# Kernel optimization log

Measured on AMD Instinct MI355X. Metric: run time of the kernel, lower is better.

## Reference

```python
import jax, jax.numpy as jnp
import numpy as np

N = 8192        # nodes
D_IN = 512      # input features
H = 256         # hidden (GAT out_features)
D_OUT = 16      # output classes
K = 16          # num clusters/classes
LRELU_SLOPE = 0.2
MASK_FILL = -9e15
EDGE_P = 0.002  # sparsity of random adjacency


def setup_inputs() -> dict:
    key = jax.random.key(0)
    k1, k2, k3, k4, k5, k6 = jax.random.split(key, 6)
    x = jax.random.normal(k1, (N, D_IN), dtype=jnp.float32)
    # binary adjacency with self loops (module only tests adj > 0; support reused as propagation matrix)
    adj = (jax.random.uniform(k2, (N, N)) < EDGE_P).astype(jnp.float32)
    adj = jnp.maximum(adj, jnp.eye(N, dtype=jnp.float32))
    C_a = jax.random.normal(k3, (K, H), dtype=jnp.float32)
    # learned parameters (xavier-ish scale)
    W = jax.random.normal(k4, (D_IN, H), dtype=jnp.float32) * (1.414 * (2.0 / (D_IN + H)) ** 0.5)
    a = jax.random.normal(k5, (2 * H, 1), dtype=jnp.float32) * (1.414 * (2.0 / (2 * H + 1)) ** 0.5)
    W_gcn = jax.random.normal(k6, (H, D_OUT), dtype=jnp.float32)
    return {"x": x, "adj": adj, "C_a": C_a, "W": W, "a": a, "W_gcn": W_gcn}


def _clust_score(Z, C):
    # score[n,k] = exp(-||Z_n - C_k||) normalized over k (beta = 1)
    d = jnp.sqrt(((Z[:, None, :] - C[None, :, :]) ** 2).sum(-1))  # [N,K]
    s = jnp.exp(-d) + 1e-10
    return s / s.sum(axis=1, keepdims=True)


def reference(x, adj, C_a, W, a, W_gcn):
    h = W.shape[1]
    # --- GAT layer ---
    Wh = x @ W                                   # [N,H]
    Wh1 = Wh @ a[:h, :]                          # [N,1]
    Wh2 = Wh @ a[h:, :]                          # [N,1]
    e = jax.nn.leaky_relu(Wh1 + Wh2.T, LRELU_SLOPE)   # [N,N]
    att = jax.nn.softmax(jnp.where(adj > 0, e, MASK_FILL), axis=1)
    Z_0 = att @ Wh                               # h_prime, [N,H]
    gatoutput = jax.nn.elu(Z_0)
    # --- cluster score on detached Z_0 (update=False path) ---
    score = _clust_score(jax.lax.stop_gradient(Z_0), C_a)
    # --- GCN layer (B_1 = I, so Z_1 = F_1) ---
    F_1 = jax.nn.relu(adj @ (gatoutput @ W_gcn))  # [N,D_OUT]
    output = F_1
    Z_1 = F_1
    return (output, Z_1, Z_0, score)
```

## Files before the change

kernel.cpp:

```cpp
#include <hip/hip_runtime.h>
#include <hip/hip_bf16.h>

#define N_NODES 8192
#define D_IN    512
#define H       256
#define D_OUT   16
#define K_CL    16
#define MAXN    96

#define OUT_OFF 0
#define Z1_OFF  131072
#define Z0_OFF  262144
#define SC_OFF  2359296

typedef unsigned int   u32;
typedef unsigned short u16;
typedef __attribute__((ext_vector_type(8))) short bf16x8;
typedef __attribute__((ext_vector_type(4))) float f32x4;

__device__ __forceinline__ float load_in(const void* p, int bf, size_t idx) {
    if (bf) { u32 w = ((const u16*)p)[idx]; return __uint_as_float(w << 16); }
    return ((const float*)p)[idx];
}
__device__ __forceinline__ void store_out(void* p, int bf, size_t idx, float v) {
    if (bf) ((__hip_bfloat16*)p)[idx] = __float2bfloat16(v);
    else    ((float*)p)[idx] = v;
}

__global__ void k_detect(const u32* __restrict__ adjw, int* __restrict__ flag) {
    int t = blockIdx.x * 256 + threadIdx.x;
    int hit = 0;
    #pragma unroll 4
    for (int i = 0; i < 16; i++)
        if (adjw[(size_t)t + (size_t)i * 65536] == 0x00003F80u) hit = 1;
    if (hit) atomicOr(flag, 1);
}

__global__ void k_prep_small(const void* av, const void* C_a, const void* Wgcn,
                             const int* __restrict__ flag,
                             float* a_f, float* Ca_f, float* Wg_f) {
    int bf = *flag;
    int i = blockIdx.x * 256 + threadIdx.x;
    if (i < 512)        a_f[i]         = load_in(av,   bf, i);
    else if (i < 4608)  Ca_f[i - 512]  = load_in(C_a,  bf, i - 512);
    else if (i < 8704)  Wg_f[i - 4608] = load_in(Wgcn, bf, i - 4608);
}

__global__ void k_prep_wt(const void* __restrict__ wraw,
                          const int* __restrict__ flag, u16* __restrict__ Wt) {
    int bf = *flag;
    int idx = blockIdx.x * 256 + threadIdx.x;
    int h = idx >> 9, k = idx & 511;
    float v = load_in(wraw, bf, (size_t)k * H + h);
    __hip_bfloat16 b = __float2bfloat16(v);
    Wt[(size_t)h * D_IN + k] = *(u16*)&b;
}

__global__ __launch_bounds__(256) void k_gemm_wh(
    const void* __restrict__ xraw, const void* __restrict__ wraw,
    const u16* __restrict__ Wt,
    const int* __restrict__ flag, float* __restrict__ Wh)
{
    int bf = *flag;
    __shared__ float xs[32][68];
    __shared__ float ws_[32][68];
    int tid = threadIdx.x;
    int bm = blockIdx.x >> 2, bn = blockIdx.x & 3;
    int m0 = bm * 64, n0 = bn * 64;

    if (bf) {
        int wave = tid >> 6, lane = tid & 63;
        int wr = wave >> 1, wc = wave & 1;
        int r0 = m0 + wr * 32, c0 = n0 + wc * 32;
        int lr = lane & 15, lk = lane >> 4;
        const u16* xp = (const u16*)xraw;
        const u16* a0p = xp + (size_t)(r0 + lr)      * D_IN + lk * 8;
        const u16* a1p = xp + (size_t)(r0 + 16 + lr) * D_IN + lk * 8;
        const u16* b0p = Wt + (size_t)(c0 + lr)      * D_IN + lk * 8;
        const u16* b1p = Wt + (size_t)(c0 + 16 + lr) * D_IN + lk * 8;
        f32x4 acc[2][2] = {};
        #pragma unroll 4
        for (int k0 = 0; k0 < D_IN; k0 += 32) {
            bf16x8 a0 = *(const bf16x8*)(a0p + k0);
            bf16x8 a1 = *(const bf16x8*)(a1p + k0);
            bf16x8 b0 = *(const bf16x8*)(b0p + k0);
            bf16x8 b1 = *(const bf16x8*)(b1p + k0);
            acc[0][0] = __builtin_amdgcn_mfma_f32_16x16x32_bf16(a0, b0, acc[0][0], 0, 0, 0);
            acc[0][1] = __builtin_amdgcn_mfma_f32_16x16x32_bf16(a0, b1, acc[0][1], 0, 0, 0);
            acc[1][0] = __builtin_amdgcn_mfma_f32_16x16x32_bf16(a1, b0, acc[1][0], 0, 0, 0);
            acc[1][1] = __builtin_amdgcn_mfma_f32_16x16x32_bf16(a1, b1, acc[1][1], 0, 0, 0);
        }
        #pragma unroll
        for (int i = 0; i < 2; i++) {
            #pragma unroll
            for (int reg = 0; reg < 4; reg++) {
                int r = r0 + 16 * i + 4 * lk + reg;
                Wh[(size_t)r * H + c0 + lr]      = acc[i][0][reg];
                Wh[(size_t)r * H + c0 + 16 + lr] = acc[i][1][reg];
            }
        }
        return;
    }

    int tx = tid & 15, ty = tid >> 4;
    float acc[4][4] = {};
    for (int k0 = 0; k0 < D_IN; k0 += 32) {
        {
            int r = tid >> 2, kq = (tid & 3) * 8;
            size_t base = (size_t)(m0 + r) * D_IN + k0 + kq;
            float4 f0 = *(const float4*)((const float*)xraw + base);
            float4 f1 = *(const float4*)((const float*)xraw + base + 4);
            xs[kq + 0][r] = f0.x; xs[kq + 1][r] = f0.y;
            xs[kq + 2][r] = f0.z; xs[kq + 3][r] = f0.w;
            xs[kq + 4][r] = f1.x; xs[kq + 5][r] = f1.y;
            xs[kq + 6][r] = f1.z; xs[kq + 7][r] = f1.w;
        }
        {
            int kk = tid >> 3, n8 = (tid & 7) * 8;
            size_t base = (size_t)(k0 + kk) * H + n0 + n8;
            float4 f0 = *(const float4*)((const float*)wraw + base);
            float4 f1 = *(const float4*)((const float*)wraw + base + 4);
            ws_[kk][n8+0]=f0.x; ws_[kk][n8+1]=f0.y; ws_[kk][n8+2]=f0.z; ws_[kk][n8+3]=f0.w;
            ws_[kk][n8+4]=f1.x; ws_[kk][n8+5]=f1.y; ws_[kk][n8+6]=f1.z; ws_[kk][n8+7]=f1.w;
        }
        __syncthreads();
        #pragma unroll
        for (int kk = 0; kk < 32; kk++) {
            float4 a4 = *(const float4*)&xs[kk][ty * 4];
            float4 b4 = *(const float4*)&ws_[kk][tx * 4];
            float a[4] = {a4.x, a4.y, a4.z, a4.w};
            float b[4] = {b4.x, b4.y, b4.z, b4.w};
            #pragma unroll
            for (int i = 0; i < 4; i++)
                #pragma unroll
                for (int j = 0; j < 4; j++)
                    acc[i][j] += a[i] * b[j];
        }
        __syncthreads();
    }
    #pragma unroll
    for (int i = 0; i < 4; i++) {
        float4 o = {acc[i][0], acc[i][1], acc[i][2], acc[i][3]};
        *(float4*)&Wh[(size_t)(m0 + ty*4 + i) * H + n0 + tx*4] = o;
    }
}

__global__ __launch_bounds__(256) void k_wh12(
    const float* __restrict__ Wh, const float* __restrict__ a_f,
    float* __restrict__ Wh1, float* __restrict__ Wh2)
{
    int tid = threadIdx.x;
    int wave = tid >> 6, lane = tid & 63;
    int n = blockIdx.x * 4 + wave;
    float4 v  = *(const float4*)(Wh + (size_t)n * H + lane * 4);
    float4 a1 = *(const float4*)(a_f + lane * 4);
    float4 a2 = *(const float4*)(a_f + H + lane * 4);
    float s1 = v.x*a1.x + v.y*a1.y + v.z*a1.z + v.w*a1.w;
    float s2 = v.x*a2.x + v.y*a2.y + v.z*a2.z + v.w*a2.w;
    #pragma unroll
    for (int off = 32; off; off >>= 1) {
        s1 += __shfl_xor(s1, off);
        s2 += __shfl_xor(s2, off);
    }
    if (lane == 0) { Wh1[n] = s1; Wh2[n] = s2; }
}

__global__ __launch_bounds__(256) void k_gat_row(
    const void* __restrict__ adjraw, const int* __restrict__ flag,
    const float* __restrict__ Wh,
    const float* __restrict__ Wh1, const float* __restrict__ Wh2,
    const float* __restrict__ Ca_f, const float* __restrict__ Wg_f,
    float* __restrict__ Gf,
    int* __restrict__ nbr_cnt, u16* __restrict__ nbr_idx,
    void* __restrict__ dout)
{
    const int n = blockIdx.x;
    const int tid = threadIdx.x;
    const int bf = *flag;
    __shared__ int   s_cnt;
    __shared__ int   s_idx[MAXN];
    __shared__ float s_att[MAXN];
    __shared__ float s_z[H];
    __shared__ float s_g[H];
    __shared__ float s_red[256];
    __shared__ float s_sc[16];

    if (tid == 0) s_cnt = 0;
    __syncthreads();

    if (bf) {
        const u16* arow = (const u16*)adjraw + (size_t)n * N_NODES;
        #pragma unroll
        for (int it = 0; it < 4; it++) {
            int base = it * 2048 + tid * 8;
            uint4 raw = *(const uint4*)(arow + base);
            u32 rw[4] = {raw.x, raw.y, raw.z, raw.w};
            #pragma unroll
            for (int q = 0; q < 4; q++) {
                #pragma unroll
                for (int hh = 0; hh < 2; hh++) {
                    u32 u = (rw[q] >> (16 * hh)) & 0xFFFFu;
                    if (__uint_as_float(u << 16) > 0.f) {
                        int p = atomicAdd(&s_cnt, 1);
                        if (p < MAXN) s_idx[p] = base + q * 2 + hh;
                    }
                }
            }
        }
    } else {
        const float* arow = (const float*)adjraw + (size_t)n * N_NODES;
        #pragma unroll
        for (int it = 0; it < 8; it++) {
            int base = it * 1024 + tid * 4;
            float4 v = *(const float4*)(arow + base);
            float vv[4] = {v.x, v.y, v.z, v.w};
            #pragma unroll
            for (int q = 0; q < 4; q++) {
                if (vv[q] > 0.f) {
                    int p = atomicAdd(&s_cnt, 1);
                    if (p < MAXN) s_idx[p] = base + q;
                }
            }
        }
    }
    __syncthreads();
    const int cnt = min(s_cnt, MAXN);
    if (tid == 0) nbr_cnt[n] = cnt;
    if (tid < cnt) nbr_idx[(size_t)n * MAXN + tid] = (u16)s_idx[tid];

    float e = 0.f;
    if (tid < cnt) {
        float v = Wh1[n] + Wh2[s_idx[tid]];
        e = v > 0.f ? v : 0.2f * v;
    }
    int lane = tid & 63, wv = tid >> 6;
    float vmax = (tid < cnt) ? e : -3e38f;
    #pragma unroll
    for (int off = 32; off; off >>= 1) vmax = fmaxf(vmax, __shfl_xor(vmax, off));
    if (lane == 0) s_red[wv] = vmax;
    __syncthreads();
    float m = fmaxf(fmaxf(s_red[0], s_red[1]), fmaxf(s_red[2], s_red[3]));
    float wexp = (tid < cnt) ? expf(e - m) : 0.f;
    float ssum = wexp;
    #pragma unroll
    for (int off = 32; off; off >>= 1) ssum += __shfl_xor(ssum, off);
    if (lane == 0) s_red[8 + wv] = ssum;
    __syncthreads();
    float denom = s_red[8] + s_red[9] + s_red[10] + s_red[11];
    if (tid < cnt) s_att[tid] = wexp / denom;
    __syncthreads();

    float acc = 0.f;
    {
        int t = 0;
        for (; t + 4 <= cnt; t += 4) {
            int i0 = s_idx[t], i1 = s_idx[t+1], i2 = s_idx[t+2], i3 = s_idx[t+3];
            float w0 = s_att[t], w1 = s_att[t+1], w2 = s_att[t+2], w3 = s_att[t+3];
            float x0 = Wh[(size_t)i0 * H + tid];
            float x1 = Wh[(size_t)i1 * H + tid];
            float x2 = Wh[(size_t)i2 * H + tid];
            float x3 = Wh[(size_t)i3 * H + tid];
            acc += w0 * x0; acc += w1 * x1; acc += w2 * x2; acc += w3 * x3;
        }
        for (; t < cnt; t++)
            acc += s_att[t] * Wh[(size_t)s_idx[t] * H + tid];
    }
    s_z[tid] = acc;
    store_out(dout, bf, (size_t)Z0_OFF + (size_t)n * H + tid, acc);
    s_g[tid] = acc > 0.f ? acc : expf(acc) - 1.f;
    __syncthreads();

    {
        int k = tid & 15, hb = (tid >> 4) * 16;
        float p = 0.f;
        #pragma unroll
        for (int i = 0; i < 16; i++) {
            float d = s_z[hb + i] - Ca_f[(size_t)k * H + hb + i];
            p += d * d;
        }
        s_red[tid] = p;
    }
    __syncthreads();
    if (tid < 16) {
        float d2 = 0.f;
        #pragma unroll
        for (int q = 0; q < 16; q++) d2 += s_red[q * 16 + tid];
        s_sc[tid] = expf(-sqrtf(d2)) + 1e-10f;
    }
    __syncthreads();
    if (tid < 16) {
        float tot = 0.f;
        #pragma unroll
        for (int q = 0; q < 16; q++) tot += s_sc[q];
        store_out(dout, bf, (size_t)SC_OFF + (size_t)n * K_CL + tid, s_sc[tid] / tot);
    }
    __syncthreads();

    {
        int o = tid & 15, hb = (tid >> 4) * 16;
        float p = 0.f;
        #pragma unroll
        for (int i = 0; i < 16; i++)
            p += s_g[hb + i] * Wg_f[(size_t)(hb + i) * D_OUT + o];
        s_red[tid] = p;
    }
    __syncthreads();
    if (tid < 16) {
        float g2 = 0.f;
        #pragma unroll
        for (int q = 0; q < 16; q++) g2 += s_red[q * 16 + tid];
        Gf[(size_t)n * D_OUT + tid] = g2;
    }
}

__global__ __launch_bounds__(256) void k_f1(
    const int* __restrict__ nbr_cnt, const u16* __restrict__ nbr_idx,
    const float* __restrict__ Gf, const int* __restrict__ flag,
    void* __restrict__ dout)
{
    int tid = threadIdx.x;
    int bf = *flag;
    int r = tid >> 4, o = tid & 15;
    int n = blockIdx.x * 16 + r;
    int cnt = nbr_cnt[n];
    const u16* idx = nbr_idx + (size_t)n * MAXN;
    float acc = 0.f;
    int t = 0;
    for (; t + 4 <= cnt; t += 4) {
        int i0 = idx[t], i1 = idx[t+1], i2 = idx[t+2], i3 = idx[t+3];
        float g0 = Gf[(size_t)i0 * D_OUT + o];
        float g1 = Gf[(size_t)i1 * D_OUT + o];
        float g2 = Gf[(size_t)i2 * D_OUT + o];
        float g3 = Gf[(size_t)i3 * D_OUT + o];
        acc += g0; acc += g1; acc += g2; acc += g3;
    }
    for (; t < cnt; t++)
        acc += Gf[(size_t)idx[t] * D_OUT + o];
    acc = fmaxf(acc, 0.f);
    store_out(dout, bf, (size_t)OUT_OFF + (size_t)n * D_OUT + o, acc);
    store_out(dout, bf, (size_t)Z1_OFF  + (size_t)n * D_OUT + o, acc);
}

extern "C" void kernel_launch(void* const* d_in, const int* in_sizes, int n_in,
                              void* d_out, int out_size, void* d_ws, size_t ws_size,
                              hipStream_t stream) {
    const void* x    = d_in[0];
    const void* adj  = d_in[1];
    const void* C_a  = d_in[2];
    const void* W    = d_in[3];
    const void* av   = d_in[4];
    const void* Wgcn = d_in[5];

    char* wsp = (char*)d_ws;
    int*   flag = (int*)wsp;                   wsp += 256;
    float* Wh   = (float*)wsp;                 wsp += (size_t)N_NODES * H * 4;
    float* Wh1  = (float*)wsp;                 wsp += (size_t)N_NODES * 4;
    float* Wh2  = (float*)wsp;                 wsp += (size_t)N_NODES * 4;
    float* Gf   = (float*)wsp;                 wsp += (size_t)N_NODES * D_OUT * 4;
    int*   ncnt = (int*)wsp;                   wsp += (size_t)N_NODES * 4;
    u16*   nidx = (u16*)wsp;                   wsp += (size_t)N_NODES * MAXN * 2;
    float* a_f  = (float*)wsp;                 wsp += 2 * H * 4;
    float* Ca_f = (float*)wsp;                 wsp += (size_t)K_CL * H * 4;
    float* Wg_f = (float*)wsp;                 wsp += (size_t)H * D_OUT * 4;
    u16*   Wt   = (u16*)wsp;                   wsp += (size_t)H * D_IN * 2;

    hipMemsetAsync(flag, 0, sizeof(int), stream);
    k_detect    <<<256, 256, 0, stream>>>((const u32*)adj, flag);
    k_prep_small<<<34, 256, 0, stream>>>(av, C_a, Wgcn, flag, a_f, Ca_f, Wg_f);
    k_prep_wt   <<<512, 256, 0, stream>>>(W, flag, Wt);
    k_gemm_wh   <<<512, 256, 0, stream>>>(x, W, Wt, flag, Wh);
    k_wh12      <<<N_NODES / 4, 256, 0, stream>>>(Wh, a_f, Wh1, Wh2);
    k_gat_row   <<<N_NODES, 256, 0, stream>>>(adj, flag, Wh, Wh1, Wh2, Ca_f, Wg_f,
                                              Gf, ncnt, nidx, d_out);
    k_f1        <<<N_NODES / 16, 256, 0, stream>>>(ncnt, nidx, Gf, flag, d_out);
}
```

Measured before the change: 443.9 us.

## Fuse prep kernels, fold Wh1/Wh2 into GEMM epilogue, drop dtype-detect kernel

Replaces the memset plus adjacency-scanning detect kernel with a one-word check of adj[0], which equals 1.0 because of the self loops. Merges the small-parameter and W-transpose prep into one kernel, using a shared-memory tiled transpose. Computes the Wh·a projections in the GEMM epilogue with shuffle reductions and atomicAdd, removing the separate k_wh12 pass over Wh. This cuts launches and memory passes, at the cost of atomic, order-dependent sums and a dtype check that depends on the diagonal entry. Also clamps the neighbor count to MAXN in k_f1.

```diff
diff --git a/kernel.cpp b/kernel.cpp
--- a/kernel.cpp
+++ b/kernel.cpp
@@ -26,42 +26,52 @@
     if (bf) ((__hip_bfloat16*)p)[idx] = __float2bfloat16(v);
     else    ((float*)p)[idx] = v;
 }
-
-__global__ void k_detect(const u32* __restrict__ adjw, int* __restrict__ flag) {
-    int t = blockIdx.x * 256 + threadIdx.x;
-    int hit = 0;
-    #pragma unroll 4
-    for (int i = 0; i < 16; i++)
-        if (adjw[(size_t)t + (size_t)i * 65536] == 0x00003F80u) hit = 1;
-    if (hit) atomicOr(flag, 1);
-}
-
-__global__ void k_prep_small(const void* av, const void* C_a, const void* Wgcn,
-                             const int* __restrict__ flag,
-                             float* a_f, float* Ca_f, float* Wg_f) {
-    int bf = *flag;
-    int i = blockIdx.x * 256 + threadIdx.x;
-    if (i < 512)        a_f[i]         = load_in(av,   bf, i);
-    else if (i < 4608)  Ca_f[i - 512]  = load_in(C_a,  bf, i - 512);
-    else if (i < 8704)  Wg_f[i - 4608] = load_in(Wgcn, bf, i - 4608);
-}
-
-__global__ void k_prep_wt(const void* __restrict__ wraw,
-                          const int* __restrict__ flag, u16* __restrict__ Wt) {
-    int bf = *flag;
-    int idx = blockIdx.x * 256 + threadIdx.x;
-    int h = idx >> 9, k = idx & 511;
-    float v = load_in(wraw, bf, (size_t)k * H + h);
-    __hip_bfloat16 b = __float2bfloat16(v);
-    Wt[(size_t)h * D_IN + k] = *(u16*)&b;
+__device__ __forceinline__ int detect_bf(const void* adj) {
+    return ((const u32*)adj)[0] != 0x3F800000u;
+}
+__device__ __forceinline__ float bf2f(u32 h) { return __uint_as_float(h << 16); }
+
+__global__ __launch_bounds__(256) void k_prep(
+    const void* __restrict__ wraw, const void* av, const void* C_a, const void* Wgcn,
+    const void* __restrict__ adj,
+    u16* __restrict__ Wt, float* a_f, float* Ca_f, float* Wg_f,
+    float* __restrict__ Wh1, float* __restrict__ Wh2)
+{
+    int bf = detect_bf(adj);
+    int b = blockIdx.x, tid = threadIdx.x;
+    if (b >= 32) {
+        int i = (b - 32) * 256 + tid;
+        if (i < 512)        a_f[i]         = load_in(av,   bf, i);
+        else if (i < 4608)  Ca_f[i - 512]  = load_in(C_a,  bf, i - 512);
+        else if (i < 8704)  Wg_f[i - 4608] = load_in(Wgcn, bf, i - 4608);
+        if (i < N_NODES) { Wh1[i] = 0.f; Wh2[i] = 0.f; }
+        return;
+    }
+    __shared__ float tile[64][65];
+    int k0 = (b >> 2) * 64, h0 = (b & 3) * 64;
+    int hh = tid & 63, kk = tid >> 6;
+    #pragma unroll
+    for (int p = 0; p < 16; p++) {
+        int k = kk * 16 + p;
+        tile[k][hh] = load_in(wraw, bf, (size_t)(k0 + k) * H + h0 + hh);
+    }
+    __syncthreads();
+    int kc = tid & 63, hr = tid >> 6;
+    #pragma unroll
+    for (int p = 0; p < 16; p++) {
+        int h = hr * 16 + p;
+        __hip_bfloat16 bb = __float2bfloat16(tile[kc][h]);
+        Wt[(size_t)(h0 + h) * D_IN + k0 + kc] = *(u16*)&bb;
+    }
 }
 
 __global__ __launch_bounds__(256) void k_gemm_wh(
     const void* __restrict__ xraw, const void* __restrict__ wraw,
-    const u16* __restrict__ Wt,
-    const int* __restrict__ flag, float* __restrict__ Wh)
+    const u16* __restrict__ Wt, const void* __restrict__ adj,
+    const float* __restrict__ a_f,
+    float* __restrict__ Wh, float* __restrict__ Wh1, float* __restrict__ Wh2)
 {
-    int bf = *flag;
+    int bf = detect_bf(adj);
     __shared__ float xs[32][68];
     __shared__ float ws_[32][68];
     int tid = threadIdx.x;
@@ -90,13 +100,27 @@
             acc[1][0] = __builtin_amdgcn_mfma_f32_16x16x32_bf16(a1, b0, acc[1][0], 0, 0, 0);
             acc[1][1] = __builtin_amdgcn_mfma_f32_16x16x32_bf16(a1, b1, acc[1][1], 0, 0, 0);
         }
+        float a1v0 = a_f[c0 + lr],     a1v1 = a_f[c0 + 16 + lr];
+        float a2v0 = a_f[H + c0 + lr], a2v1 = a_f[H + c0 + 16 + lr];
         #pragma unroll
         for (int i = 0; i < 2; i++) {
             #pragma unroll
             for (int reg = 0; reg < 4; reg++) {
                 int r = r0 + 16 * i + 4 * lk + reg;
-                Wh[(size_t)r * H + c0 + lr]      = acc[i][0][reg];
-                Wh[(size_t)r * H + c0 + 16 + lr] = acc[i][1][reg];
+                float v0 = acc[i][0][reg], v1 = acc[i][1][reg];
+                Wh[(size_t)r * H + c0 + lr]      = v0;
+                Wh[(size_t)r * H + c0 + 16 + lr] = v1;
+                float s1 = a1v0 * v0 + a1v1 * v1;
+                float s2 = a2v0 * v0 + a2v1 * v1;
+                #pragma unroll
+                for (int off = 8; off; off >>= 1) {
+                    s1 += __shfl_xor(s1, off);
+                    s2 += __shfl_xor(s2, off);
+                }
+                if (lr == 0) {
+                    atomicAdd(&Wh1[r], s1);
+                    atomicAdd(&Wh2[r], s2);
+                }
             }
         }
         return;
@@ -138,35 +162,28 @@
         }
         __syncthreads();
     }
+    float4 av1 = *(const float4*)(a_f + n0 + tx * 4);
+    float4 av2 = *(const float4*)(a_f + H + n0 + tx * 4);
     #pragma unroll
     for (int i = 0; i < 4; i++) {
         float4 o = {acc[i][0], acc[i][1], acc[i][2], acc[i][3]};
         *(float4*)&Wh[(size_t)(m0 + ty*4 + i) * H + n0 + tx*4] = o;
-    }
-}
-
-__global__ __launch_bounds__(256) void k_wh12(
-    const float* __restrict__ Wh, const float* __restrict__ a_f,
-    float* __restrict__ Wh1, float* __restrict__ Wh2)
-{
-    int tid = threadIdx.x;
-    int wave = tid >> 6, lane = tid & 63;
-    int n = blockIdx.x * 4 + wave;
-    float4 v  = *(const float4*)(Wh + (size_t)n * H + lane * 4);
-    float4 a1 = *(const float4*)(a_f + lane * 4);
-    float4 a2 = *(const float4*)(a_f + H + lane * 4);
-    float s1 = v.x*a1.x + v.y*a1.y + v.z*a1.z + v.w*a1.w;
-    float s2 = v.x*a2.x + v.y*a2.y + v.z*a2.z + v.w*a2.w;
-    #pragma unroll
-    for (int off = 32; off; off >>= 1) {
-        s1 += __shfl_xor(s1, off);
-        s2 += __shfl_xor(s2, off);
-    }
-    if (lane == 0) { Wh1[n] = s1; Wh2[n] = s2; }
+        float s1 = o.x*av1.x + o.y*av1.y + o.z*av1.z + o.w*av1.w;
+        float s2 = o.x*av2.x + o.y*av2.y + o.z*av2.z + o.w*av2.w;
+        #pragma unroll
+        for (int off = 8; off; off >>= 1) {
+            s1 += __shfl_xor(s1, off);
+            s2 += __shfl_xor(s2, off);
+        }
+        if (tx == 0) {
+            atomicAdd(&Wh1[m0 + ty*4 + i], s1);
+            atomicAdd(&Wh2[m0 + ty*4 + i], s2);
+        }
+    }
 }
 
 __global__ __launch_bounds__(256) void k_gat_row(
-    const void* __restrict__ adjraw, const int* __restrict__ flag,
+    const void* __restrict__ adjraw,
     const float* __restrict__ Wh,
     const float* __restrict__ Wh1, const float* __restrict__ Wh2,
     const float* __restrict__ Ca_f, const float* __restrict__ Wg_f,
@@ -176,7 +193,7 @@
 {
     const int n = blockIdx.x;
     const int tid = threadIdx.x;
-    const int bf = *flag;
+    const int bf = detect_bf(adjraw);
     __shared__ int   s_cnt;
     __shared__ int   s_idx[MAXN];
     __shared__ float s_att[MAXN];
@@ -200,7 +217,7 @@
                 #pragma unroll
                 for (int hh = 0; hh < 2; hh++) {
                     u32 u = (rw[q] >> (16 * hh)) & 0xFFFFu;
-                    if (__uint_as_float(u << 16) > 0.f) {
+                    if (bf2f(u) > 0.f) {
                         int p = atomicAdd(&s_cnt, 1);
                         if (p < MAXN) s_idx[p] = base + q * 2 + hh;
                     }
@@ -315,14 +332,14 @@
 
 __global__ __launch_bounds__(256) void k_f1(
     const int* __restrict__ nbr_cnt, const u16* __restrict__ nbr_idx,
-    const float* __restrict__ Gf, const int* __restrict__ flag,
+    const float* __restrict__ Gf, const void* __restrict__ adj,
     void* __restrict__ dout)
 {
     int tid = threadIdx.x;
-    int bf = *flag;
+    int bf = detect_bf(adj);
     int r = tid >> 4, o = tid & 15;
     int n = blockIdx.x * 16 + r;
-    int cnt = nbr_cnt[n];
+    int cnt = min(nbr_cnt[n], MAXN);
     const u16* idx = nbr_idx + (size_t)n * MAXN;
     float acc = 0.f;
     int t = 0;
@@ -352,7 +369,6 @@
     const void* Wgcn = d_in[5];
 
     char* wsp = (char*)d_ws;
-    int*   flag = (int*)wsp;                   wsp += 256;
     float* Wh   = (float*)wsp;                 wsp += (size_t)N_NODES * H * 4;
     float* Wh1  = (float*)wsp;                 wsp += (size_t)N_NODES * 4;
     float* Wh2  = (float*)wsp;                 wsp += (size_t)N_NODES * 4;
@@ -364,13 +380,10 @@
     float* Wg_f = (float*)wsp;                 wsp += (size_t)H * D_OUT * 4;
     u16*   Wt   = (u16*)wsp;                   wsp += (size_t)H * D_IN * 2;
 
-    hipMemsetAsync(flag, 0, sizeof(int), stream);
-    k_detect    <<<256, 256, 0, stream>>>((const u32*)adj, flag);
-    k_prep_small<<<34, 256, 0, stream>>>(av, C_a, Wgcn, flag, a_f, Ca_f, Wg_f);
-    k_prep_wt   <<<512, 256, 0, stream>>>(W, flag, Wt);
-    k_gemm_wh   <<<512, 256, 0, stream>>>(x, W, Wt, flag, Wh);
-    k_wh12      <<<N_NODES / 4, 256, 0, stream>>>(Wh, a_f, Wh1, Wh2);
-    k_gat_row   <<<N_NODES, 256, 0, stream>>>(adj, flag, Wh, Wh1, Wh2, Ca_f, Wg_f,
-                                              Gf, ncnt, nidx, d_out);
-    k_f1        <<<N_NODES / 16, 256, 0, stream>>>(ncnt, nidx, Gf, flag, d_out);
-}
+    k_prep    <<<66, 256, 0, stream>>>(W, av, C_a, Wgcn, adj, Wt, a_f, Ca_f, Wg_f,
+                                       Wh1, Wh2);
+    k_gemm_wh <<<512, 256, 0, stream>>>(x, W, Wt, adj, a_f, Wh, Wh1, Wh2);
+    k_gat_row <<<N_NODES, 256, 0, stream>>>(adj, Wh, Wh1, Wh2, Ca_f, Wg_f,
+                                            Gf, ncnt, nidx, d_out);
+    k_f1      <<<N_NODES / 16, 256, 0, stream>>>(ncnt, nidx, Gf, adj, d_out);
+}
```

Result: no change. 442.8 us (-0.2%).
